# Kernel tuning notes

Hardware: AMD Instinct MI355X
Metric: run time of the kernel (lower is better)

The kernel has to match this reference:

```python
import jax, jax.numpy as jnp
import numpy as np
from jax.ops import segment_sum

N_NODES, N_EDGES, FEAT, HID, LAT = 50000, 800000, 128, 64, 32
NUM_GRAPHS, MAX_NODES = 64, 30


def setup_inputs() -> dict:
    key = jax.random.key(0)
    ks = jax.random.split(key, 24)
    def lin(k, fi, fo):
        kw, kb = jax.random.split(k)
        s = 1.0 / np.sqrt(fi)
        return (jax.random.uniform(kw, (fi, fo), jnp.float32, -s, s),
                jax.random.uniform(kb, (fo,), jnp.float32, -s, s))
    W1, b1 = lin(ks[0], FEAT, HID)
    W2, b2 = lin(ks[1], HID, HID)
    Wmu, bmu = lin(ks[2], HID, LAT)
    Wlv, blv = lin(ks[3], HID, LAT)
    Wl1, bl1 = lin(ks[4], LAT, HID)
    Wl2, bl2 = lin(ks[5], HID, HID * MAX_NODES)
    We1, be1 = lin(ks[6], 2 * HID, HID)
    We2, be2 = lin(ks[7], HID, 1)
    x = jax.random.normal(ks[8], (N_NODES, FEAT), jnp.float32)
    edge_index = jax.random.randint(ks[9], (2, N_EDGES), 0, N_NODES, jnp.int64)
    batch = jnp.sort(jax.random.randint(ks[10], (N_NODES,), 0, NUM_GRAPHS, jnp.int64))
    return {"x": x, "edge_index": edge_index, "batch": batch, "num_nodes": MAX_NODES,
            "W1": W1, "b1": b1, "W2": W2, "b2": b2, "Wmu": Wmu, "bmu": bmu,
            "Wlv": Wlv, "blv": blv, "Wl1": Wl1, "bl1": bl1, "Wl2": Wl2, "bl2": bl2,
            "We1": We1, "be1": be1, "We2": We2, "be2": be2}


def reference(x, edge_index, batch, num_nodes, W1, b1, W2, b2, Wmu, bmu,
              Wlv, blv, Wl1, bl1, Wl2, bl2, We1, be1, We2, be2):
    N = x.shape[0]
    src, dst = edge_index[0], edge_index[1]
    # GCN normalization with self-loops: deg over A+I
    deg = segment_sum(jnp.ones_like(src, jnp.float32), dst, num_segments=N) + 1.0
    dinv = jax.lax.rsqrt(deg)
    enorm = dinv[src] * dinv[dst]            # [E]
    snorm = dinv * dinv                      # self-loop norm [N]

    def gcn(h, W, b):
        h = h @ W                            # transform before gather (smaller)
        agg = segment_sum(h[src] * enorm[:, None], dst, num_segments=N)
        return agg + h * snorm[:, None] + b

    h = jax.nn.relu(gcn(x, W1, b1))
    h = jax.nn.relu(gcn(h, W2, b2))

    counts = segment_sum(jnp.ones((N,), jnp.float32), batch, num_segments=NUM_GRAPHS)
    pooled = segment_sum(h, batch, num_segments=NUM_GRAPHS) / jnp.maximum(counts, 1.0)[:, None]
    mu = pooled @ Wmu + bmu
    logvar = pooled @ Wlv + blv
    z = mu  # eval-mode reparameterize

    node_emb = (jax.nn.relu(z @ Wl1 + bl1) @ Wl2 + bl2).reshape(NUM_GRAPHS, MAX_NODES, HID)
    emb = node_emb[0, :num_nodes]            # [n, HID]
    Wtop, Wbot = We1[:HID], We1[HID:]
    hi = emb @ Wtop                          # [n, HID]
    hj = emb @ Wbot
    hidp = jax.nn.relu(hi[:, None, :] + hj[None, :, :] + be1)  # [n, n, HID]
    probs = jax.nn.sigmoid((hidp @ We2)[..., 0] + be2[0])       # [n, n]
    upper = jnp.triu(probs, k=1)
    adj = upper + upper.T
    return adj, mu, logvar
```

## Files before the change

### kernel.cpp

```cpp
#include <hip/hip_runtime.h>
#include <hip/hip_bf16.h>
#include <math.h>

#define FEAT 128
#define HID 64
#define LAT 32
#define NG 64
#define MAXN 30
#define NPART 8
#define CAP 64
#define FILLB 2048

typedef __hip_bfloat16 bf16;
typedef short bf16x8 __attribute__((ext_vector_type(8)));
typedef float f32x4 __attribute__((ext_vector_type(4)));

__global__ void k_zero_conv(int* p, int nzero, int zb,
                            const float* __restrict__ W1,
                            const float* __restrict__ W2,
                            bf16* __restrict__ w1t,
                            bf16* __restrict__ w2t) {
    int tid = threadIdx.x;
    if ((int)blockIdx.x < zb) {
        int i = blockIdx.x * 256 + tid;
        if (i < nzero) p[i] = 0;
        return;
    }
    int idx = (blockIdx.x - zb) * 256 + tid;
    if (idx < FEAT * HID) {
        int k = idx >> 6, f = idx & 63;
        w1t[f * FEAT + k] = __float2bfloat16(W1[idx]);
    } else if (idx < FEAT * HID + HID * HID) {
        int r = idx - FEAT * HID;
        int k = r >> 6, f = r & 63;
        w2t[f * HID + k] = __float2bfloat16(W2[r]);
    }
}

__global__ __launch_bounds__(256) void k_fill_gemm(const int* __restrict__ src,
                                                   const int* __restrict__ dst,
                                                   int* __restrict__ cnt,
                                                   unsigned short* __restrict__ slots,
                                                   const float* __restrict__ x,
                                                   const bf16* __restrict__ w1t,
                                                   bf16* __restrict__ hw,
                                                   int N, int E) {
    __shared__ __align__(16) bf16 X[16][136];
    int tid = threadIdx.x;
    if (blockIdx.x < FILLB) {
        int part = blockIdx.x & (NPART - 1);
        int psz0 = (N + NPART - 1) / NPART;
        int base = part * psz0;
        int psize = min(psz0, N - base);
        int bi = blockIdx.x >> 3;
        const long stride = (long)(FILLB >> 3) * 256;
        for (long e = (long)bi * 256 + tid; e < E; e += stride) {
            int d = dst[e];
            int r = d - base;
            if ((unsigned)r < (unsigned)psize) {
                int pos = atomicAdd(&cnt[d], 1);
                if (pos < CAP) slots[((long)d << 6) + pos] = (unsigned short)src[e];
            }
        }
        return;
    }
    int gblk = blockIdx.x - FILLB;
    int r0 = gblk * 16;
    {
        int kw = tid & 63;
        int rr = tid >> 6;
        for (int r = rr; r < 16; r += 4) {
            int row = r0 + r;
            float x0 = 0.f, x1 = 0.f;
            if (row < N) {
                const float* xp = x + (long)row * FEAT + 2 * kw;
                x0 = xp[0];
                x1 = xp[1];
            }
            __hip_bfloat162 p;
            p.x = __float2bfloat16(x0);
            p.y = __float2bfloat16(x1);
            *(__hip_bfloat162*)&X[r][2 * kw] = p;
        }
    }
    __syncthreads();
    int wv = tid >> 6, lane = tid & 63;
    int m = lane & 15;
    int kb = (lane >> 4) * 8;
    int f0 = wv * 16;
    const bf16* wrow = w1t + (f0 + m) * FEAT;
    f32x4 acc = {0.f, 0.f, 0.f, 0.f};
#pragma unroll
    for (int t = 0; t < 4; ++t) {
        bf16x8 a = *reinterpret_cast<const bf16x8*>(&X[m][kb + 32 * t]);
        bf16x8 bb = *reinterpret_cast<const bf16x8*>(wrow + kb + 32 * t);
        acc = __builtin_amdgcn_mfma_f32_16x16x32_bf16(a, bb, acc, 0, 0, 0);
    }
#pragma unroll
    for (int rg = 0; rg < 4; ++rg) {
        int row = (lane >> 4) * 4 + rg;
        int nid = r0 + row;
        if (nid < N) hw[((long)nid << 6) + f0 + m] = __float2bfloat16(acc[rg]);
    }
}

__device__ inline void red4(float4& a) {
    a.x += __shfl_xor(a.x, 16); a.y += __shfl_xor(a.y, 16);
    a.z += __shfl_xor(a.z, 16); a.w += __shfl_xor(a.w, 16);
    a.x += __shfl_xor(a.x, 32); a.y += __shfl_xor(a.y, 32);
    a.z += __shfl_xor(a.z, 32); a.w += __shfl_xor(a.w, 32);
}

#define ACC4(v, en)                                              \
    acc.x += __uint_as_float(((v).x & 0xFFFFu) << 16) * (en);    \
    acc.y += __uint_as_float((v).x & 0xFFFF0000u) * (en);        \
    acc.z += __uint_as_float(((v).y & 0xFFFFu) << 16) * (en);    \
    acc.w += __uint_as_float((v).y & 0xFFFF0000u) * (en);

__device__ inline float4 gather_core(const bf16* __restrict__ hw,
                                     const unsigned short* __restrict__ slots,
                                     const int* __restrict__ cnt,
                                     int wid, int cntv, float di, int lane,
                                     const float* __restrict__ b) {
    int sub = lane >> 4, q = lane & 15;
    long j0 = (long)wid << 6;
    float4 acc = make_float4(0.f, 0.f, 0.f, 0.f);
    int s_r = wid;
    float en_r = 0.0f;
    if (lane < cntv) {
        s_r = slots[j0 + lane];
        en_r = rsqrtf(1.0f + (float)cnt[s_r]) * di;
    }
    int nld = (cntv + 3) >> 2;
    uint2 v[16];
#pragma unroll
    for (int l = 0; l < 16; ++l) {
        if (l < nld) {
            int s = __shfl(s_r, l * 4 + sub);
            v[l] = *reinterpret_cast<const uint2*>(hw + (((long)s << 6) + (q << 2)));
        }
    }
#pragma unroll
    for (int l = 0; l < 16; ++l) {
        if (l < nld) {
            float en = __shfl(en_r, l * 4 + sub);
            ACC4(v[l], en);
        }
    }
    red4(acc);
    uint2 sv = *reinterpret_cast<const uint2*>(hw + (((long)wid << 6) + (q << 2)));
    float sn = di * di;
    float4 bq = *reinterpret_cast<const float4*>(b + (q << 2));
    acc.x += __uint_as_float((sv.x & 0xFFFFu) << 16) * sn + bq.x;
    acc.y += __uint_as_float(sv.x & 0xFFFF0000u) * sn + bq.y;
    acc.z += __uint_as_float((sv.y & 0xFFFFu) << 16) * sn + bq.z;
    acc.w += __uint_as_float(sv.y & 0xFFFF0000u) * sn + bq.w;
    return acc;
}

__global__ __launch_bounds__(1024) void k_gather_mm(const bf16* __restrict__ hw,
                                                    const unsigned short* __restrict__ slots,
                                                    const int* __restrict__ cnt,
                                                    const float* __restrict__ b1,
                                                    const bf16* __restrict__ w2t,
                                                    bf16* __restrict__ hw2, int N) {
    __shared__ __align__(16) bf16 H[16][72];
    int tid = threadIdx.x;
    int wv = tid >> 6, lane = tid & 63;
    int wid = blockIdx.x * 16 + wv;
    if (wid < N) {
        int c_full = cnt[wid];
        int cntv = min(c_full, CAP);
        float di = rsqrtf(1.0f + (float)c_full);
        float4 r = gather_core(hw, slots, cnt, wid, cntv, di, lane, b1);
        if (lane < 16) {
            int c = lane << 2;
            H[wv][c + 0] = __float2bfloat16(fmaxf(r.x, 0.f));
            H[wv][c + 1] = __float2bfloat16(fmaxf(r.y, 0.f));
            H[wv][c + 2] = __float2bfloat16(fmaxf(r.z, 0.f));
            H[wv][c + 3] = __float2bfloat16(fmaxf(r.w, 0.f));
        }
    }
    __syncthreads();
    if (wv < 4) {
        int m = lane & 15;
        int kb = (lane >> 4) * 8;
        int f0 = wv * 16;
        const bf16* wrow = w2t + (f0 + m) * HID;
        bf16x8 a0 = *reinterpret_cast<const bf16x8*>(&H[m][kb]);
        bf16x8 a1 = *reinterpret_cast<const bf16x8*>(&H[m][kb + 32]);
        bf16x8 b0 = *reinterpret_cast<const bf16x8*>(wrow + kb);
        bf16x8 b1f = *reinterpret_cast<const bf16x8*>(wrow + kb + 32);
        f32x4 acc = {0.f, 0.f, 0.f, 0.f};
        acc = __builtin_amdgcn_mfma_f32_16x16x32_bf16(a0, b0, acc, 0, 0, 0);
        acc = __builtin_amdgcn_mfma_f32_16x16x32_bf16(a1, b1f, acc, 0, 0, 0);
#pragma unroll
        for (int rg = 0; rg < 4; ++rg) {
            int row = (lane >> 4) * 4 + rg;
            int nid = blockIdx.x * 16 + row;
            if (nid < N) hw2[((long)nid << 6) + f0 + m] = __float2bfloat16(acc[rg]);
        }
    }
}

__global__ __launch_bounds__(256) void k_gather4(const bf16* __restrict__ hw,
                                                 const unsigned short* __restrict__ slots,
                                                 const int* __restrict__ cnt,
                                                 const float* __restrict__ b,
                                                 float* __restrict__ outb, int N) {
    int wv = threadIdx.x >> 6, lane = threadIdx.x & 63;
    int wid = blockIdx.x * 4 + wv;
    if (wid >= N) return;
    int c_full = cnt[wid];
    int cntv = min(c_full, CAP);
    float di = rsqrtf(1.0f + (float)c_full);
    float4 r = gather_core(hw, slots, cnt, wid, cntv, di, lane, b);
    if ((lane >> 4) == 0)
        *reinterpret_cast<float4*>(outb + (((long)wid << 6) + ((lane & 15) << 2))) = r;
}

__global__ __launch_bounds__(256) void k_relu_pool(const float* __restrict__ agg,
                                                   const int* __restrict__ batch,
                                                   float* __restrict__ pooled,
                                                   float* __restrict__ counts,
                                                   int N, int rows_per_wave) {
    int wid = blockIdx.x * (blockDim.x >> 6) + (threadIdx.x >> 6);
    int lane = threadIdx.x & 63;
    int i0 = wid * rows_per_wave;
    if (i0 >= N) return;
    int i1 = min(i0 + rows_per_wave, N);
    int cur = batch[i0];
    float acc = 0.0f, cnt = 0.0f;
    for (int i = i0; i < i1; ++i) {
        int g = batch[i];
        if (g != cur) {
            atomicAdd(&pooled[cur * 64 + lane], acc);
            if (lane == 0) atomicAdd(&counts[cur], cnt);
            acc = 0.0f; cnt = 0.0f; cur = g;
        }
        acc += fmaxf(agg[(long)i * 64 + lane], 0.0f);
        cnt += 1.0f;
    }
    atomicAdd(&pooled[cur * 64 + lane], acc);
    if (lane == 0) atomicAdd(&counts[cur], cnt);
}

__global__ __launch_bounds__(256) void k_heads_dec1(const float* __restrict__ pooled,
                                                    const float* __restrict__ counts,
                                                    const float* __restrict__ Wmu,
                                                    const float* __restrict__ bmu,
                                                    const float* __restrict__ Wlv,
                                                    const float* __restrict__ blv,
                                                    const float* __restrict__ Wl1,
                                                    const float* __restrict__ bl1,
                                                    const float* __restrict__ Wl2,
                                                    const float* __restrict__ bl2,
                                                    const float* __restrict__ We1,
                                                    float* __restrict__ out,
                                                    float* __restrict__ hi,
                                                    float* __restrict__ hj) {
    int blk = blockIdx.x;
    int tid = threadIdx.x;
    if (blk < MAXN) {
        __shared__ float prow[HID];
        __shared__ float z0[LAT];
        __shared__ float hr[HID];
        __shared__ float em[HID];
        int n = blk;
        if (tid < HID) prow[tid] = pooled[tid];
        __syncthreads();
        if (tid < LAT) {
            float c0 = fmaxf(counts[0], 1.0f);
            float s = 0.0f;
#pragma unroll 8
            for (int h = 0; h < HID; ++h) s += prow[h] * Wmu[h * 32 + tid];
            z0[tid] = s / c0 + bmu[tid];
        }
        __syncthreads();
        if (tid < HID) {
            float s = bl1[tid];
#pragma unroll
            for (int l = 0; l < LAT; ++l) s += z0[l] * Wl1[l * HID + tid];
            hr[tid] = fmaxf(s, 0.0f);
        }
        __syncthreads();
        if (tid < HID) {
            float e = bl2[n * HID + tid];
#pragma unroll 8
            for (int h = 0; h < HID; ++h) e += hr[h] * Wl2[h * (HID * MAXN) + n * HID + tid];
            em[tid] = e;
        }
        __syncthreads();
        if (tid < HID) {
            float a = 0.0f, bb = 0.0f;
#pragma unroll 8
            for (int f = 0; f < HID; ++f) {
                float ev = em[f];
                a += ev * We1[f * HID + tid];
                bb += ev * We1[(HID + f) * HID + tid];
            }
            hi[n * HID + tid] = a;
            hj[n * HID + tid] = bb;
        }
    } else {
        int idx = (blk - MAXN) * 256 + tid;
        int which = idx >> 11;
        int r = idx & (NG * LAT - 1);
        int g = r >> 5, l = r & 31;
        const float* W = which ? Wlv : Wmu;
        const float* b = which ? blv : bmu;
        float s = 0.0f;
#pragma unroll 8
        for (int h = 0; h < HID; ++h) s += pooled[g * 64 + h] * W[h * 32 + l];
        float c = fmaxf(counts[g], 1.0f);
        out[900 + idx] = s / c + b[l];
    }
}

__global__ __launch_bounds__(256) void k_dec2(const float* __restrict__ hi,
                                              const float* __restrict__ hj,
                                              const float* __restrict__ be1,
                                              const float* __restrict__ We2,
                                              const float* __restrict__ be2,
                                              float* __restrict__ out) {
    __shared__ float shi[MAXN * 65];
    __shared__ float shj[MAXN * 65];
    __shared__ float sbe[HID];
    __shared__ float sw[HID];
    int tid = threadIdx.x;
    for (int i = tid; i < MAXN * HID; i += 256) {
        int n = i >> 6, k = i & 63;
        shi[n * 65 + k] = hi[i];
        shj[n * 65 + k] = hj[i];
    }
    if (tid < HID) { sbe[tid] = be1[tid]; sw[tid] = We2[tid]; }
    __syncthreads();
    float bias2 = be2[0];
    for (int idx = tid; idx < MAXN * MAXN; idx += 256) {
        int i = idx / MAXN, j = idx % MAXN;
        if (i == j) { out[idx] = 0.0f; continue; }
        int a = i < j ? i : j;
        int b = i < j ? j : i;
        float s = bias2;
#pragma unroll 8
        for (int k = 0; k < HID; ++k)
            s += fmaxf(shi[a * 65 + k] + shj[b * 65 + k] + sbe[k], 0.0f) * sw[k];
        out[idx] = 1.0f / (1.0f + expf(-s));
    }
}

extern "C" void kernel_launch(void* const* d_in, const int* in_sizes, int n_in,
                              void* d_out, int out_size, void* d_ws, size_t ws_size,
                              hipStream_t stream) {
    const float* x = (const float*)d_in[0];
    const int* ei = (const int*)d_in[1];
    const int* batch = (const int*)d_in[2];
    const float* W1 = (const float*)d_in[4];
    const float* b1 = (const float*)d_in[5];
    const float* W2 = (const float*)d_in[6];
    const float* b2 = (const float*)d_in[7];
    const float* Wmu = (const float*)d_in[8];
    const float* bmu = (const float*)d_in[9];
    const float* Wlv = (const float*)d_in[10];
    const float* blv = (const float*)d_in[11];
    const float* Wl1 = (const float*)d_in[12];
    const float* bl1 = (const float*)d_in[13];
    const float* Wl2 = (const float*)d_in[14];
    const float* bl2 = (const float*)d_in[15];
    const float* We1 = (const float*)d_in[16];
    const float* be1 = (const float*)d_in[17];
    const float* We2 = (const float*)d_in[18];
    const float* be2 = (const float*)d_in[19];

    const int N = in_sizes[2];
    const int E = in_sizes[1] / 2;
    const int* src = ei;
    const int* dst = ei + E;

    char* ws = (char*)d_ws;
    size_t off_b = 0;
    auto alloc = [&](size_t nbytes) {
        void* p = (void*)(ws + off_b);
        off_b = (off_b + nbytes + 255) & ~(size_t)255;
        return p;
    };
    float* bufA   = (float*)alloc((size_t)N * 64 * 4);
    bf16*  hwb1   = (bf16*)alloc((size_t)N * 64 * 2);
    bf16*  hwb2   = (bf16*)alloc((size_t)N * 64 * 2);
    const int nzero = N + NG * HID + NG;
    int*   cnt    = (int*)alloc((size_t)nzero * 4);
    float* pooled = (float*)(cnt + N);
    float* counts = pooled + NG * HID;
    unsigned short* slots = (unsigned short*)alloc((size_t)N * CAP * 2);
    bf16*  w1t    = (bf16*)alloc(FEAT * HID * 2);
    bf16*  w2t    = (bf16*)alloc(HID * HID * 2);
    float* dhi    = (float*)alloc(MAXN * HID * 4);
    float* dhj    = (float*)alloc(MAXN * HID * 4);

    float* out = (float*)d_out;

    const int zb = (nzero + 255) / 256;
    const int cvb = (FEAT * HID + HID * HID + 255) / 256;
    k_zero_conv<<<zb + cvb, 256, 0, stream>>>(cnt, nzero, zb, W1, W2, w1t, w2t);

    k_fill_gemm<<<FILLB + (N + 15) / 16, 256, 0, stream>>>(src, dst, cnt, slots,
                                                           x, w1t, hwb1, N, E);

    k_gather_mm<<<(N + 15) / 16, 1024, 0, stream>>>(hwb1, slots, cnt, b1, w2t, hwb2, N);

    k_gather4<<<(N + 3) / 4, 256, 0, stream>>>(hwb2, slots, cnt, b2, bufA, N);

    {
        const int waves = 2048;
        int rpw = (N + waves - 1) / waves;
        k_relu_pool<<<512, 256, 0, stream>>>(bufA, batch, pooled, counts, N, rpw);
    }

    k_heads_dec1<<<MAXN + 16, 256, 0, stream>>>(pooled, counts, Wmu, bmu, Wlv, blv,
                                                Wl1, bl1, Wl2, bl2, We1, out, dhi, dhj);

    k_dec2<<<1, 256, 0, stream>>>(dhi, dhj, be1, We2, be2, out);
}
```

Baseline: 143.6 us.

## Fuse second GCN gather with ReLU mean-pool and interleave fill/GEMM blocks

The second-layer gather now applies ReLU and accumulates each block's four node rows into the per-graph pooled sums through shared memory and atomics. This removes the full fp32 N×64 intermediate buffer and the separate pool kernel launch. The fill_gemm grid is also rearranged so edge-bucketing blocks and x@W1 GEMM blocks are interleaved in a 2:3 ratio per group of eight blocks, with the partition tied to the XCD index, so the two kinds of work overlap instead of running in sequence. The cost is more atomics on pooled, roughly one set per block instead of per wave-chunk, and the fill stride changes from 256 to 262 blocks.

Measured after the change: 203.0 us. 41.4% more time.

```diff
diff --git a/kernel.cpp b/kernel.cpp
--- a/kernel.cpp
+++ b/kernel.cpp
@@ -9,7 +9,8 @@
 #define MAXN 30
 #define NPART 8
 #define CAP 64
-#define FILLB 2048
+#define T_OCT 655
+#define FILL_OCT 262
 
 typedef __hip_bfloat16 bf16;
 typedef short bf16x8 __attribute__((ext_vector_type(8)));
@@ -47,13 +48,14 @@
                                                    int N, int E) {
     __shared__ __align__(16) bf16 X[16][136];
     int tid = threadIdx.x;
-    if (blockIdx.x < FILLB) {
-        int part = blockIdx.x & (NPART - 1);
+    int o = blockIdx.x >> 3;
+    int xcd = blockIdx.x & 7;
+    if (o % 5 < 2) {
+        int bi = (o / 5) * 2 + (o % 5);
         int psz0 = (N + NPART - 1) / NPART;
-        int base = part * psz0;
+        int base = xcd * psz0;
         int psize = min(psz0, N - base);
-        int bi = blockIdx.x >> 3;
-        const long stride = (long)(FILLB >> 3) * 256;
+        const long stride = (long)FILL_OCT * 256;
         for (long e = (long)bi * 256 + tid; e < E; e += stride) {
             int d = dst[e];
             int r = d - base;
@@ -64,7 +66,9 @@
         }
         return;
     }
-    int gblk = blockIdx.x - FILLB;
+    int go = (o / 5) * 3 + (o % 5) - 2;
+    int gblk = go * 8 + xcd;
+    if (gblk >= (N + 15) / 16) return;
     int r0 = gblk * 16;
     {
         int kw = tid & 63;
@@ -203,46 +207,52 @@
     }
 }
 
-__global__ __launch_bounds__(256) void k_gather4(const bf16* __restrict__ hw,
-                                                 const unsigned short* __restrict__ slots,
-                                                 const int* __restrict__ cnt,
-                                                 const float* __restrict__ b,
-                                                 float* __restrict__ outb, int N) {
+__global__ __launch_bounds__(256) void k_gather_pool2(const bf16* __restrict__ hw,
+                                                      const unsigned short* __restrict__ slots,
+                                                      const int* __restrict__ cnt,
+                                                      const float* __restrict__ b,
+                                                      const int* __restrict__ batch,
+                                                      float* __restrict__ pooled,
+                                                      float* __restrict__ counts,
+                                                      int N) {
+    __shared__ float rows[4][64];
+    __shared__ int gid[4];
     int wv = threadIdx.x >> 6, lane = threadIdx.x & 63;
     int wid = blockIdx.x * 4 + wv;
-    if (wid >= N) return;
-    int c_full = cnt[wid];
-    int cntv = min(c_full, CAP);
-    float di = rsqrtf(1.0f + (float)c_full);
-    float4 r = gather_core(hw, slots, cnt, wid, cntv, di, lane, b);
-    if ((lane >> 4) == 0)
-        *reinterpret_cast<float4*>(outb + (((long)wid << 6) + ((lane & 15) << 2))) = r;
-}
-
-__global__ __launch_bounds__(256) void k_relu_pool(const float* __restrict__ agg,
-                                                   const int* __restrict__ batch,
-                                                   float* __restrict__ pooled,
-                                                   float* __restrict__ counts,
-                                                   int N, int rows_per_wave) {
-    int wid = blockIdx.x * (blockDim.x >> 6) + (threadIdx.x >> 6);
-    int lane = threadIdx.x & 63;
-    int i0 = wid * rows_per_wave;
-    if (i0 >= N) return;
-    int i1 = min(i0 + rows_per_wave, N);
-    int cur = batch[i0];
-    float acc = 0.0f, cnt = 0.0f;
-    for (int i = i0; i < i1; ++i) {
-        int g = batch[i];
-        if (g != cur) {
+    if (wid < N) {
+        int c_full = cnt[wid];
+        int cntv = min(c_full, CAP);
+        float di = rsqrtf(1.0f + (float)c_full);
+        float4 r = gather_core(hw, slots, cnt, wid, cntv, di, lane, b);
+        if ((lane >> 4) == 0) {
+            r.x = fmaxf(r.x, 0.f); r.y = fmaxf(r.y, 0.f);
+            r.z = fmaxf(r.z, 0.f); r.w = fmaxf(r.w, 0.f);
+            *reinterpret_cast<float4*>(&rows[wv][(lane & 15) << 2]) = r;
+        }
+        if (lane == 0) gid[wv] = batch[wid];
+    } else {
+        if (lane == 0) gid[wv] = -1;
+    }
+    __syncthreads();
+    if (wv == 0) {
+        float acc = 0.0f, cf = 0.0f;
+        int cur = gid[0];
+        for (int t = 0; t < 4; ++t) {
+            int g = gid[t];
+            if (g < 0) break;
+            if (g != cur) {
+                atomicAdd(&pooled[cur * 64 + lane], acc);
+                if (lane == 0) atomicAdd(&counts[cur], cf);
+                acc = 0.0f; cf = 0.0f; cur = g;
+            }
+            acc += rows[t][lane];
+            cf += 1.0f;
+        }
+        if (cur >= 0) {
             atomicAdd(&pooled[cur * 64 + lane], acc);
-            if (lane == 0) atomicAdd(&counts[cur], cnt);
-            acc = 0.0f; cnt = 0.0f; cur = g;
-        }
-        acc += fmaxf(agg[(long)i * 64 + lane], 0.0f);
-        cnt += 1.0f;
-    }
-    atomicAdd(&pooled[cur * 64 + lane], acc);
-    if (lane == 0) atomicAdd(&counts[cur], cnt);
+            if (lane == 0) atomicAdd(&counts[cur], cf);
+        }
+    }
 }
 
 __global__ __launch_bounds__(256) void k_heads_dec1(const float* __restrict__ pooled,
@@ -384,7 +394,6 @@
         off_b = (off_b + nbytes + 255) & ~(size_t)255;
         return p;
     };
-    float* bufA   = (float*)alloc((size_t)N * 64 * 4);
     bf16*  hwb1   = (bf16*)alloc((size_t)N * 64 * 2);
     bf16*  hwb2   = (bf16*)alloc((size_t)N * 64 * 2);
     const int nzero = N + NG * HID + NG;
@@ -403,18 +412,13 @@
     const int cvb = (FEAT * HID + HID * HID + 255) / 256;
     k_zero_conv<<<zb + cvb, 256, 0, stream>>>(cnt, nzero, zb, W1, W2, w1t, w2t);
 
-    k_fill_gemm<<<FILLB + (N + 15) / 16, 256, 0, stream>>>(src, dst, cnt, slots,
-                                                           x, w1t, hwb1, N, E);
+    k_fill_gemm<<<T_OCT * 8, 256, 0, stream>>>(src, dst, cnt, slots,
+                                               x, w1t, hwb1, N, E);
 
     k_gather_mm<<<(N + 15) / 16, 1024, 0, stream>>>(hwb1, slots, cnt, b1, w2t, hwb2, N);
 
-    k_gather4<<<(N + 3) / 4, 256, 0, stream>>>(hwb2, slots, cnt, b2, bufA, N);
-
-    {
-        const int waves = 2048;
-        int rpw = (N + waves - 1) / waves;
-        k_relu_pool<<<512, 256, 0, stream>>>(bufA, batch, pooled, counts, N, rpw);
-    }
+    k_gather_pool2<<<(N + 3) / 4, 256, 0, stream>>>(hwb2, slots, cnt, b2, batch,
+                                                    pooled, counts, N);
 
     k_heads_dec1<<<MAXN + 16, 256, 0, stream>>>(pooled, counts, Wmu, bmu, Wlv, blv,
                                                 Wl1, bl1, Wl2, bl2, We1, out, dhi, dhj);
```
